# Kernel tuning notes

Hardware: AMD Instinct MI355X
Metric: run time of the kernel (lower is better)

## Reference

```python
import jax, jax.numpy as jnp
import numpy as np
import math

D_MODEL = 256
D_STATE = 16
D_CONV = 4
EXPAND = 2
N_HEADS = 4
D_INNER = EXPAND * D_MODEL          # 512
DT_RANK = (D_MODEL + 15) // 16      # 16
B_SZ, SEQ = 4, 2048


def setup_inputs() -> dict:
    key = jax.random.key(0)
    ks = jax.random.split(key, 12)
    rn = lambda i, shp, sc=0.02: jax.random.normal(ks[i], shp, dtype=jnp.float32) * sc
    x = jax.random.normal(ks[0], (B_SZ, SEQ, D_MODEL), dtype=jnp.float32)
    return dict(
        x=x,
        ln_g=jnp.ones((D_MODEL,), jnp.float32),
        ln_b=jnp.zeros((D_MODEL,), jnp.float32),
        W_in=rn(1, (D_MODEL, 2 * D_INNER)),
        conv_w=rn(2, (D_INNER, D_CONV), 0.1),
        conv_b=jnp.zeros((D_INNER,), jnp.float32),
        W_xproj=rn(3, (D_INNER, DT_RANK + 2 * D_STATE)),
        W_dt=rn(4, (DT_RANK, D_INNER), 0.1),
        b_dt=jnp.full((D_INNER,), -4.6, jnp.float32),  # softplus ~ 0.01 init
        A_log=jnp.log(jnp.tile(jnp.arange(1, D_STATE + 1, dtype=jnp.float32), (D_INNER, 1))),
        Dp=jnp.ones((D_INNER,), jnp.float32),
        W_out_m=rn(5, (D_INNER, D_MODEL)),
        W_qkv=rn(6, (D_MODEL, 3 * D_MODEL)),
        b_qkv=jnp.zeros((3 * D_MODEL,), jnp.float32),
        W_o=rn(7, (D_MODEL, D_MODEL)),
        b_o=jnp.zeros((D_MODEL,), jnp.float32),
        W_gate=rn(8, (2 * D_MODEL, D_MODEL)),
        b_gate=jnp.zeros((D_MODEL,), jnp.float32),
    )


def _sssd_forward(x, ln_g, ln_b, W_in, conv_w, conv_b, W_xproj, W_dt, b_dt,
                  A_log, Dp, W_out_m, W_qkv, b_qkv, W_o, b_o, W_gate, b_gate):
    B, L, D = x.shape
    # LayerNorm
    mu = x.mean(-1, keepdims=True)
    var = x.var(-1, keepdims=True)
    xn = (x - mu) * jax.lax.rsqrt(var + 1e-5) * ln_g + ln_b

    # ---- Mamba branch ----
    xz = xn @ W_in                      # (B,L,2*D_INNER)
    xm, z = jnp.split(xz, 2, axis=-1)
    # causal depthwise conv1d (kernel D_CONV)
    xp = jnp.pad(xm, ((0, 0), (D_CONV - 1, 0), (0, 0)))
    xc = conv_b + sum(xp[:, k:k + L, :] * conv_w[:, k] for k in range(D_CONV))
    xc = jax.nn.silu(xc)
    dbl = xc @ W_xproj                  # (B,L,DT_RANK+2*D_STATE)
    dt_in = dbl[..., :DT_RANK]
    Bm = dbl[..., DT_RANK:DT_RANK + D_STATE]
    Cm = dbl[..., DT_RANK + D_STATE:]
    dt = jax.nn.softplus(dt_in @ W_dt + b_dt)   # (B,L,D_INNER)
    A = -jnp.exp(A_log)                 # (D_INNER, D_STATE)

    def step(h, inp):
        x_t, dt_t, B_t, C_t = inp       # (B,Din),(B,Din),(B,N),(B,N)
        dA = jnp.exp(dt_t[..., None] * A)               # (B,Din,N)
        h = dA * h + (dt_t * x_t)[..., None] * B_t[:, None, :]
        y = jnp.einsum('bdn,bn->bd', h, C_t)
        return h, y

    h0 = jnp.zeros((B, D_INNER, D_STATE), x.dtype)
    xs = (jnp.swapaxes(xc, 0, 1), jnp.swapaxes(dt, 0, 1),
          jnp.swapaxes(Bm, 0, 1), jnp.swapaxes(Cm, 0, 1))
    _, ys = jax.lax.scan(step, h0, xs)
    y = jnp.swapaxes(ys, 0, 1) + xc * Dp
    y = y * jax.nn.silu(z)
    ssm_out = y @ W_out_m               # (B,L,D)

    # ---- MHSA branch (eval: no dropout) ----
    hd = D // N_HEADS
    qkv = xn @ W_qkv + b_qkv
    q, k, v = jnp.split(qkv, 3, axis=-1)
    sh = lambda t: t.reshape(B, L, N_HEADS, hd).transpose(0, 2, 1, 3)
    q, k, v = sh(q), sh(k), sh(v)
    scores = jnp.einsum('bhqd,bhkd->bhqk', q, k) * (1.0 / math.sqrt(hd))
    attn = jax.nn.softmax(scores, axis=-1)
    o = jnp.einsum('bhqk,bhkd->bhqd', attn, v).transpose(0, 2, 1, 3).reshape(B, L, D)
    attn_out = o @ W_o + b_o

    # ---- sigmoid gate fusion ----
    gate = jax.nn.sigmoid(jnp.concatenate([ssm_out, attn_out], axis=-1) @ W_gate + b_gate)
    fused = gate * ssm_out + (1.0 - gate) * attn_out
    return x + fused


def reference(x, ln_g, ln_b, W_in, conv_w, conv_b, W_xproj, W_dt, b_dt,
              A_log, Dp, W_out_m, W_qkv, b_qkv, W_o, b_o, W_gate, b_gate):
    return _sssd_forward(x, ln_g, ln_b, W_in, conv_w, conv_b, W_xproj, W_dt, b_dt,
                         A_log, Dp, W_out_m, W_qkv, b_qkv, W_o, b_o, W_gate, b_gate)
```

## Files before the change

### kernel.cpp

```cpp
#include <hip/hip_runtime.h>
#include <math.h>

#define B_SZ 4
#define SEQ 2048
#define DM 256
#define DI 512
#define DS 16
#define DTR 16
#define NH 4
#define HD 64
#define T_TOK (B_SZ*SEQ)
#define NCH 64
#define CL (SEQ/NCH)
#define QSCALE 0.18033688f

typedef short bf16x8 __attribute__((ext_vector_type(8)));
typedef float f32x4  __attribute__((ext_vector_type(4)));
typedef unsigned short u16;

__device__ __forceinline__ float sigmoidf_(float x){ return 1.f/(1.f+__expf(-x)); }
__device__ __forceinline__ u16 f2bf(float x){
  unsigned int u = __float_as_uint(x);
  u += 0x7fffu + ((u>>16)&1u);
  return (u16)(u>>16);
}
__device__ __forceinline__ float bf2f(u16 u){ return __uint_as_float(((unsigned)u)<<16); }
__device__ __forceinline__ unsigned cvt_pk_bf16(float lo, float hi){
  unsigned r;
  asm("v_cvt_pk_bf16_f32 %0, %1, %2" : "=v"(r) : "v"(lo), "v"(hi));
  return r;
}

struct TcvtArgs {
  const float* src[6];
  u16* dst[6];
  int K[6];
  int Nvalid[6];
  int Npad[6];
};
__global__ __launch_bounds__(256) void tcvt_all(TcvtArgs a) {
  int wi = blockIdx.z;
  int K = a.K[wi], Nv = a.Nvalid[wi], Np = a.Npad[wi];
  int k0 = blockIdx.x*64, n0 = blockIdx.y*64;
  if (k0 >= K || n0 >= Np) return;
  __shared__ u16 tile[64][65];
  const float* src = a.src[wi];
  u16* dst = a.dst[wi];
  int tn = threadIdx.x & 63, tq = threadIdx.x >> 6;
#pragma unroll
  for (int j=0;j<16;++j){
    int kk = j*4 + tq;
    int n = n0 + tn;
    tile[tn][kk] = (n < Nv) ? f2bf(src[(size_t)(k0+kk)*Nv + n]) : (u16)0;
  }
  __syncthreads();
#pragma unroll
  for (int j=0;j<16;++j){
    int nn = j*4 + tq;
    dst[(size_t)(n0+nn)*K + k0 + tn] = tile[nn][tn];
  }
}

__global__ __launch_bounds__(256) void ln_kernel(const float* __restrict__ x,
    const float* __restrict__ g, const float* __restrict__ b,
    u16* __restrict__ xn_bf) {
  int wid = threadIdx.x >> 6;
  int lane = threadIdx.x & 63;
  int token = blockIdx.x*4 + wid;
  const float* xr = x + (size_t)token*DM;
  float4 v = *(const float4*)&xr[lane*4];
  float s  = v.x+v.y+v.z+v.w;
  float ss = v.x*v.x+v.y*v.y+v.z*v.z+v.w*v.w;
  for (int m=1;m<64;m<<=1){ s += __shfl_xor(s,m); ss += __shfl_xor(ss,m); }
  float mu  = s * (1.f/DM);
  float var = ss*(1.f/DM) - mu*mu;
  float rs  = rsqrtf(var + 1e-5f);
  float4 gv = *(const float4*)&g[lane*4];
  float4 bv = *(const float4*)&b[lane*4];
  uint2 o;
  o.x = cvt_pk_bf16((v.x-mu)*rs*gv.x + bv.x, (v.y-mu)*rs*gv.y + bv.y);
  o.y = cvt_pk_bf16((v.z-mu)*rs*gv.z + bv.z, (v.w-mu)*rs*gv.w + bv.w);
  *(uint2*)&xn_bf[(size_t)token*DM + lane*4] = o;
}

template<int ACT>
__global__ __launch_bounds__(256) void gemm_mfma(const u16* __restrict__ A,
    const u16* __restrict__ Wt, const float* __restrict__ bias,
    float* __restrict__ C, u16* __restrict__ Cbf, int K, int ldc, int nvalid,
    int qcols, float qscale, const float* __restrict__ xres,
    const float* __restrict__ cat2, u16* __restrict__ vTout) {
  __shared__ u16 lds[12288];
  int tid = threadIdx.x;
  int m0 = blockIdx.y*128, n0 = blockIdx.x*64;
  int w = tid>>6, l = tid&63, lq = l&15, lg = l>>4;
  int wm = w>>1, wn = w&1;
  f32x4 acc[4][2] = {};
  for (int k0 = 0; k0 < K; k0 += 64) {
#pragma unroll
    for (int i=0;i<4;++i){
      int gid = i*256 + tid;
      int row = gid>>3, g = gid&7;
      *(bf16x8*)&lds[row*64 + ((g ^ (row&7))*8)] =
          *(const bf16x8*)&A[(size_t)(m0+row)*K + k0 + g*8];
    }
#pragma unroll
    for (int i=0;i<2;++i){
      int gid = i*256 + tid;
      int row = gid>>3, g = gid&7;
      *(bf16x8*)&lds[8192 + row*64 + ((g ^ (row&7))*8)] =
          *(const bf16x8*)&Wt[(size_t)(n0+row)*K + k0 + g*8];
    }
    __syncthreads();
#pragma unroll
    for (int ks=0;ks<2;++ks){
      bf16x8 af[4], bfv[2];
#pragma unroll
      for (int mi=0;mi<4;++mi){
        int row = wm*64 + mi*16 + lq;
        af[mi] = *(bf16x8*)&lds[row*64 + (((ks*4+lg) ^ (row&7))*8)];
      }
#pragma unroll
      for (int nj=0;nj<2;++nj){
        int row = wn*32 + nj*16 + lq;
        bfv[nj] = *(bf16x8*)&lds[8192 + row*64 + (((ks*4+lg) ^ (row&7))*8)];
      }
#pragma unroll
      for (int mi=0;mi<4;++mi)
#pragma unroll
        for (int nj=0;nj<2;++nj)
          acc[mi][nj] = __builtin_amdgcn_mfma_f32_16x16x32_bf16(af[mi], bfv[nj], acc[mi][nj], 0,0,0);
    }
    __syncthreads();
  }
#pragma unroll
  for (int mi=0;mi<4;++mi){
#pragma unroll
    for (int nj=0;nj<2;++nj){
#pragma unroll
      for (int r=0;r<4;++r){
        int row = m0 + wm*64 + mi*16 + lg*4 + r;
        int col = n0 + wn*32 + nj*16 + lq;
        if (col < nvalid) {
          float v = acc[mi][nj][r];
          if (bias) v += bias[col];
          if (col < qcols) v *= qscale;
          if (ACT==2) {
            float g = sigmoidf_(v);
            float sv = cat2[(size_t)row*512 + col];
            float av = cat2[(size_t)row*512 + 256 + col];
            C[(size_t)row*256 + col] = xres[(size_t)row*256 + col] + g*sv + (1.f-g)*av;
          } else if (ACT==3) {
            Cbf[(size_t)row*ldc + col] = f2bf(v);
            if (col >= 512) {
              int bb = row>>11, ll = row&2047;
              int hh = (col-512)>>6, dd = (col-512)&63;
              vTout[(((size_t)(bb*4+hh))*64 + dd)*SEQ + ll] = f2bf(v);
            }
          } else {
            if (ACT==1) v = sigmoidf_(v);
            if (C)   C[(size_t)row*ldc + col] = v;
            if (Cbf) Cbf[(size_t)row*ldc + col] = f2bf(v);
          }
        }
      }
    }
  }
}

__global__ __launch_bounds__(256) void conv_kernel(const u16* __restrict__ xzb,
    const float* __restrict__ cw, const float* __restrict__ cb,
    u16* __restrict__ xc_bf) {
  int idx = blockIdx.x*256 + threadIdx.x;
  int d2 = (idx & 255)*2;
  int t = idx >> 8;
  int l = t & (SEQ-1);
  float acc0 = cb[d2], acc1 = cb[d2+1];
  float4 wA = *(const float4*)&cw[d2*4];
  float4 wB = *(const float4*)&cw[d2*4+4];
  const u16* base = xzb + (size_t)t*1024 + d2;
  ushort2 v;
  if (l>=3){ v = *(const ushort2*)&base[-3*1024]; acc0 += bf2f(v.x)*wA.x; acc1 += bf2f(v.y)*wB.x; }
  if (l>=2){ v = *(const ushort2*)&base[-2*1024]; acc0 += bf2f(v.x)*wA.y; acc1 += bf2f(v.y)*wB.y; }
  if (l>=1){ v = *(const ushort2*)&base[-1*1024]; acc0 += bf2f(v.x)*wA.z; acc1 += bf2f(v.y)*wB.z; }
  v = *(const ushort2*)&base[0];
  acc0 += bf2f(v.x)*wA.w; acc1 += bf2f(v.y)*wB.w;
  float r0 = acc0 * sigmoidf_(acc0);
  float r1 = acc1 * sigmoidf_(acc1);
  *(unsigned*)&xc_bf[(size_t)t*DI + d2] = cvt_pk_bf16(r0, r1);
}

__global__ __launch_bounds__(256) void dt_kernel(const float* __restrict__ dbl,
    const float* __restrict__ Wdt, const float* __restrict__ bdt,
    float* __restrict__ dt) {
  __shared__ float sdbl[4][16];
  int wid = threadIdx.x>>6, lane = threadIdx.x&63;
  int token = blockIdx.x*4 + wid;
  if (lane < 16) sdbl[wid][lane] = dbl[(size_t)token*48 + lane];
  __syncthreads();
  float din[16];
#pragma unroll
  for (int k=0;k<16;++k) din[k] = sdbl[wid][k];
#pragma unroll
  for (int r=0;r<8;++r){
    int d = lane + r*64;
    float acc = bdt[d];
#pragma unroll
    for (int k=0;k<16;++k) acc += din[k]*Wdt[k*DI+d];
    float sp = (acc > 20.f) ? acc : log1pf(__expf(acc));
    dt[(size_t)token*DI+d] = sp;
  }
}

__global__ __launch_bounds__(512) void scan_p1(const u16* __restrict__ xc_bf,
    const float* __restrict__ dt, const float* __restrict__ dbl,
    const float* __restrict__ A_log, float* __restrict__ Pws, float* __restrict__ Hws) {
  __shared__ float sB[CL][16];
  int d = threadIdx.x;
  int bc = blockIdx.x;
  int b = bc >> 6, c = bc & 63;
  {
    int t = threadIdx.x >> 4, n = threadIdx.x & 15;
    sB[t][n] = dbl[((size_t)b*SEQ + c*CL + t)*48 + DTR + n];
  }
  __syncthreads();
  float An[16];
#pragma unroll
  for (int i=0;i<4;++i){
    float4 a = *(const float4*)&A_log[d*16 + i*4];
    An[i*4+0] = -__expf(a.x); An[i*4+1] = -__expf(a.y);
    An[i*4+2] = -__expf(a.z); An[i*4+3] = -__expf(a.w);
  }
  float h[16] = {};
  float P[16];
#pragma unroll
  for (int n=0;n<16;++n) P[n] = 1.f;
  size_t tok = (size_t)b*SEQ + c*CL;
  for (int t=0;t<CL;++t,++tok){
    float dtv = dt[tok*DI+d];
    float xcv = bf2f(xc_bf[tok*DI+d]);
    float u = dtv*xcv;
    float4 B0 = *(float4*)&sB[t][0];
    float4 B1 = *(float4*)&sB[t][4];
    float4 B2 = *(float4*)&sB[t][8];
    float4 B3 = *(float4*)&sB[t][12];
    float Bv[16] = {B0.x,B0.y,B0.z,B0.w,B1.x,B1.y,B1.z,B1.w,
                    B2.x,B2.y,B2.z,B2.w,B3.x,B3.y,B3.z,B3.w};
#pragma unroll
    for (int n=0;n<16;++n){
      float e = __expf(dtv*An[n]);
      P[n] *= e;
      h[n] = e*h[n] + u*Bv[n];
    }
  }
  size_t base = (((size_t)b*NCH + c)*DI + d)*16;
#pragma unroll
  for (int n=0;n<16;++n){ Pws[base+n] = P[n]; Hws[base+n] = h[n]; }
}

__global__ __launch_bounds__(256) void scan_combine(const float* __restrict__ Pws,
    const float* __restrict__ Hws, float* __restrict__ H0ws) {
  int gid = blockIdx.x*256 + threadIdx.x;
  int b  = gid >> 13;
  int dn = gid & 8191;
  float h0 = 0.f;
#pragma unroll 4
  for (int c=0;c<NCH;++c){
    size_t idx = ((size_t)(b*NCH+c)<<13) + dn;
    H0ws[idx] = h0;
    h0 = Pws[idx]*h0 + Hws[idx];
  }
}

__global__ __launch_bounds__(512) void scan_p2(const u16* __restrict__ xc_bf,
    const float* __restrict__ dt, const float* __restrict__ dbl,
    const float* __restrict__ A_log, const float* __restrict__ Dp,
    const u16* __restrict__ xzb, const float* __restrict__ H0ws,
    u16* __restrict__ ygate_bf) {
  __shared__ float sBC[CL][32];
  int d = threadIdx.x;
  int bc = blockIdx.x;
  int b = bc >> 6, c = bc & 63;
#pragma unroll
  for (int i=0;i<2;++i){
    int idx = i*512 + threadIdx.x;
    int t = idx >> 5, q = idx & 31;
    sBC[t][q] = dbl[((size_t)b*SEQ + c*CL + t)*48 + DTR + q];
  }
  __syncthreads();
  float An[16];
#pragma unroll
  for (int i=0;i<4;++i){
    float4 a = *(const float4*)&A_log[d*16 + i*4];
    An[i*4+0] = -__expf(a.x); An[i*4+1] = -__expf(a.y);
    An[i*4+2] = -__expf(a.z); An[i*4+3] = -__expf(a.w);
  }
  float Dd = Dp[d];
  float h[16];
  size_t base = (((size_t)b*NCH + c)*DI + d)*16;
#pragma unroll
  for (int i=0;i<4;++i){
    float4 h4 = *(const float4*)&H0ws[base + i*4];
    h[i*4+0]=h4.x; h[i*4+1]=h4.y; h[i*4+2]=h4.z; h[i*4+3]=h4.w;
  }
  size_t tok = (size_t)b*SEQ + c*CL;
  for (int t=0;t<CL;++t,++tok){
    float dtv = dt[tok*DI+d];
    float xcv = bf2f(xc_bf[tok*DI+d]);
    float zv  = bf2f(xzb[tok*1024 + DI + d]);
    float u = dtv*xcv;
    float4 B0 = *(float4*)&sBC[t][0];
    float4 B1 = *(float4*)&sBC[t][4];
    float4 B2 = *(float4*)&sBC[t][8];
    float4 B3 = *(float4*)&sBC[t][12];
    float4 C0 = *(float4*)&sBC[t][16];
    float4 C1 = *(float4*)&sBC[t][20];
    float4 C2 = *(float4*)&sBC[t][24];
    float4 C3 = *(float4*)&sBC[t][28];
    float Bv[16] = {B0.x,B0.y,B0.z,B0.w,B1.x,B1.y,B1.z,B1.w,
                    B2.x,B2.y,B2.z,B2.w,B3.x,B3.y,B3.z,B3.w};
    float Cv[16] = {C0.x,C0.y,C0.z,C0.w,C1.x,C1.y,C1.z,C1.w,
                    C2.x,C2.y,C2.z,C2.w,C3.x,C3.y,C3.z,C3.w};
    float y = 0.f;
#pragma unroll
    for (int n=0;n<16;++n){
      float e = __expf(dtv*An[n]);
      h[n] = e*h[n] + u*Bv[n];
      y += h[n]*Cv[n];
    }
    y += xcv*Dd;
    ygate_bf[tok*DI + d] = f2bf(y * (zv*sigmoidf_(zv)));
  }
}

__global__ __launch_bounds__(256) void attn_mfma_kernel(const u16* __restrict__ qkvb,
    const u16* __restrict__ vT,
    float* __restrict__ Opart, float* __restrict__ ml) {
  __shared__ u16 lds[24576];
  int H = blockIdx.x + 16*blockIdx.y + 256*(int)blockIdx.z;
  int cx = H & 7, k = H >> 3;
  int xq = k & 15;
  int G  = cx*8 + (k >> 4);
  int bh = G & 15, s = G >> 4;
  int b = bh>>2, h = bh&3;
  int tid = threadIdx.x;
  int w = tid>>6, l = tid&63;
  int lq = l & 15;
  int lg = l >> 4;
  size_t bbase = (size_t)b*SEQ;
  size_t vbase = (size_t)bh*HD*SEQ;
  int q0 = xq*128 + w*32;

  bf16x8 qf[2][2];
#pragma unroll
  for (int qg=0; qg<2; ++qg)
#pragma unroll
    for (int dsl=0; dsl<2; ++dsl)
      qf[qg][dsl] = *(const bf16x8*)&qkvb[(bbase + q0 + qg*16 + lq)*768 + h*HD + lg*8 + dsl*32];

  float m_[2] = {-1e30f,-1e30f}, l_[2] = {0.f,0.f};
  f32x4 oacc[2][4] = {};
  int pbase = 16384 + w*2048;

  int srow = tid>>3, sg = tid&7;
  int kt0 = s*8;
  bf16x8 kreg[2], vreg[2];

#define LOADT(kt) { \
  kreg[0] = *(const bf16x8*)&qkvb[(bbase + (size_t)(kt)*64 + srow)*768 + 256 + h*HD + sg*8]; \
  kreg[1] = *(const bf16x8*)&qkvb[(bbase + (size_t)(kt)*64 + srow + 32)*768 + 256 + h*HD + sg*8]; \
  vreg[0] = *(const bf16x8*)&vT[vbase + (size_t)srow*SEQ + (kt)*64 + sg*8]; \
  vreg[1] = *(const bf16x8*)&vT[vbase + (size_t)(srow+32)*SEQ + (kt)*64 + sg*8]; }
#define STORET(bi) { \
  *(bf16x8*)&lds[(bi)*4096 + srow*64 + ((sg ^ (srow&7))*8)] = kreg[0]; \
  *(bf16x8*)&lds[(bi)*4096 + (srow+32)*64 + ((sg ^ ((srow+32)&7))*8)] = kreg[1]; \
  *(bf16x8*)&lds[8192 + (bi)*4096 + srow*64 + ((sg ^ (srow&7))*8)] = vreg[0]; \
  *(bf16x8*)&lds[8192 + (bi)*4096 + (srow+32)*64 + ((sg ^ ((srow+32)&7))*8)] = vreg[1]; }

  LOADT(kt0);
  STORET(0);
  __syncthreads();
  int cur = 0;

  for (int it=0; it<8; ++it){
    if (it < 7) LOADT(kt0+it+1);

    int kb = cur*4096, vb = 8192 + cur*4096;
    f32x4 sacc[2][4] = {};
    __builtin_amdgcn_s_setprio(1);
#pragma unroll
    for (int kg=0;kg<4;++kg){
#pragma unroll
      for (int dsl=0;dsl<2;++dsl){
        int row = kg*16 + lq;
        bf16x8 kf = *(bf16x8*)&lds[kb + row*64 + (((dsl*4 + lg) ^ (row&7))*8)];
        sacc[0][kg] = __builtin_amdgcn_mfma_f32_16x16x32_bf16(kf, qf[0][dsl], sacc[0][kg], 0,0,0);
        sacc[1][kg] = __builtin_amdgcn_mfma_f32_16x16x32_bf16(kf, qf[1][dsl], sacc[1][kg], 0,0,0);
      }
    }
    __builtin_amdgcn_s_setprio(0);

#pragma unroll
    for (int qg=0;qg<2;++qg){
      float tm = sacc[qg][0][0];
#pragma unroll
      for (int kg=0;kg<4;++kg){
        float a = fmaxf(fmaxf(sacc[qg][kg][0],sacc[qg][kg][1]),
                        fmaxf(sacc[qg][kg][2],sacc[qg][kg][3]));
        tm = fmaxf(tm, a);
      }
      tm = fmaxf(tm, __shfl_xor(tm,16));
      tm = fmaxf(tm, __shfl_xor(tm,32));
      if (__any(tm - m_[qg] > 8.f)) {
        float mn = fmaxf(m_[qg], tm);
        float sc = exp2f(m_[qg] - mn);
        m_[qg] = mn;
        l_[qg] *= sc;
#pragma unroll
        for (int dg=0;dg<4;++dg){
          oacc[qg][dg][0]*=sc; oacc[qg][dg][1]*=sc; oacc[qg][dg][2]*=sc; oacc[qg][dg][3]*=sc;
        }
      }
      float ps = 0.f;
#pragma unroll
      for (int kg=0;kg<4;++kg){
        float p0 = exp2f(sacc[qg][kg][0] - m_[qg]);
        float p1 = exp2f(sacc[qg][kg][1] - m_[qg]);
        float p2 = exp2f(sacc[qg][kg][2] - m_[qg]);
        float p3 = exp2f(sacc[qg][kg][3] - m_[qg]);
        ps += (p0+p1)+(p2+p3);
        int off = pbase + qg*1024 + lq*64 + (((2*kg + (lg>>1)) ^ (lq&7))*8) + 4*(lg&1);
        *(unsigned*)&lds[off]   = cvt_pk_bf16(p0, p1);
        *(unsigned*)&lds[off+2] = cvt_pk_bf16(p2, p3);
      }
      ps += __shfl_xor(ps,16);
      ps += __shfl_xor(ps,32);
      l_[qg] += ps;
    }

    __builtin_amdgcn_s_setprio(1);
#pragma unroll
    for (int ks=0;ks<2;++ks){
      bf16x8 pf0 = *(bf16x8*)&lds[pbase        + lq*64 + (((ks*4 + lg) ^ (lq&7))*8)];
      bf16x8 pf1 = *(bf16x8*)&lds[pbase + 1024 + lq*64 + (((ks*4 + lg) ^ (lq&7))*8)];
#pragma unroll
      for (int dg=0;dg<4;++dg){
        int row = dg*16 + lq;
        bf16x8 vf = *(bf16x8*)&lds[vb + row*64 + (((ks*4 + lg) ^ (row&7))*8)];
        oacc[0][dg] = __builtin_amdgcn_mfma_f32_16x16x32_bf16(vf, pf0, oacc[0][dg], 0,0,0);
        oacc[1][dg] = __builtin_amdgcn_mfma_f32_16x16x32_bf16(vf, pf1, oacc[1][dg], 0,0,0);
      }
    }
    __builtin_amdgcn_s_setprio(0);

    if (it < 7) STORET(cur^1);
    __syncthreads();
    cur ^= 1;
  }
#undef LOADT
#undef STORET

  int sidx = bh*4 + s;
#pragma unroll
  for (int qg=0;qg<2;++qg){
    size_t rb = ((size_t)sidx*SEQ + q0 + qg*16 + lq)*64;
#pragma unroll
    for (int dg=0;dg<4;++dg)
#pragma unroll
      for (int r=0;r<4;++r)
        Opart[rb + dg*16 + lg*4 + r] = oacc[qg][dg][r];
    if (lg==0){
      ml[((size_t)sidx*SEQ + q0 + qg*16 + lq)*2    ] = m_[qg];
      ml[((size_t)sidx*SEQ + q0 + qg*16 + lq)*2 + 1] = l_[qg];
    }
  }
}

__global__ __launch_bounds__(256) void attn_merge_kernel(const float* __restrict__ Opart,
    const float* __restrict__ ml, u16* __restrict__ attn_bf) {
  int w = threadIdx.x>>6, lane = threadIdx.x&63;
  int R = blockIdx.x*4 + w;
  int bh = R>>11, q = R&2047;
  float m[4], lv[4];
#pragma unroll
  for (int s=0;s<4;++s){
    m[s]  = ml[((size_t)(bh*4+s)*SEQ + q)*2];
    lv[s] = ml[((size_t)(bh*4+s)*SEQ + q)*2 + 1];
  }
  float ms = fmaxf(fmaxf(m[0],m[1]),fmaxf(m[2],m[3]));
  float o = 0.f, lsum = 0.f;
#pragma unroll
  for (int s=0;s<4;++s){
    float wsc = exp2f(m[s]-ms);
    lsum += wsc*lv[s];
    o += wsc*Opart[((size_t)(bh*4+s)*SEQ + q)*64 + lane];
  }
  size_t token = (size_t)(bh>>2)*SEQ + q;
  attn_bf[token*DM + (bh&3)*HD + lane] = f2bf(o/lsum);
}

extern "C" void kernel_launch(void* const* d_in, const int* in_sizes, int n_in,
                              void* d_out, int out_size, void* d_ws, size_t ws_size,
                              hipStream_t stream) {
  const float* x      = (const float*)d_in[0];
  const float* ln_g   = (const float*)d_in[1];
  const float* ln_b   = (const float*)d_in[2];
  const float* W_in   = (const float*)d_in[3];
  const float* conv_w = (const float*)d_in[4];
  const float* conv_b = (const float*)d_in[5];
  const float* W_xproj= (const float*)d_in[6];
  const float* W_dt   = (const float*)d_in[7];
  const float* b_dt   = (const float*)d_in[8];
  const float* A_log  = (const float*)d_in[9];
  const float* Dp     = (const float*)d_in[10];
  const float* W_out_m= (const float*)d_in[11];
  const float* W_qkv  = (const float*)d_in[12];
  const float* b_qkv  = (const float*)d_in[13];
  const float* W_o    = (const float*)d_in[14];
  const float* b_o    = (const float*)d_in[15];
  const float* W_gate = (const float*)d_in[16];
  const float* b_gate = (const float*)d_in[17];
  float* out = (float*)d_out;

  float* ws = (float*)d_ws;
  u16*   xn_bf   = (u16*)(ws);
  u16*   xzb     = (u16*)(ws + 1048576);
  u16*   qkv_bf  = (u16*)(ws + 9437184);
  u16*   xc_bf   = (u16*)(ws + 12582912);
  float* dblb    = ws + 16777216;
  float* dtb     = ws + 17170432;
  u16*   ygate_bf= (u16*)(ws + 21364736);
  u16*   attn_bf = (u16*)(ws + 23461888);
  float* catb    = ws + 24510464;
  u16*   catb_bf = (u16*)(ws + 28704768);
  float* gateb   = ws + 30801920;
  u16*   Wt_all  = (u16*)(ws + 32899072);
  float* Opart = ws + 1048576;
  float* mlb   = (float*)xn_bf;
  u16*   vTb   = (u16*)gateb;
  float* Pws   = catb;
  float* Hws   = catb + 2097152;
  float* H0ws  = catb + 4194304;

  u16* Wt_in   = Wt_all;
  u16* Wt_qkv  = Wt_all + 262144;
  u16* Wt_out  = Wt_all + 458752;
  u16* Wt_o    = Wt_all + 589824;
  u16* Wt_gate = Wt_all + 655360;
  u16* Wt_xp   = Wt_all + 786432;

  TcvtArgs ta;
  ta.src[0]=W_in;    ta.dst[0]=Wt_in;   ta.K[0]=256; ta.Nvalid[0]=1024; ta.Npad[0]=1024;
  ta.src[1]=W_qkv;   ta.dst[1]=Wt_qkv;  ta.K[1]=256; ta.Nvalid[1]=768;  ta.Npad[1]=768;
  ta.src[2]=W_out_m; ta.dst[2]=Wt_out;  ta.K[2]=512; ta.Nvalid[2]=256;  ta.Npad[2]=256;
  ta.src[3]=W_o;     ta.dst[3]=Wt_o;    ta.K[3]=256; ta.Nvalid[3]=256;  ta.Npad[3]=256;
  ta.src[4]=W_gate;  ta.dst[4]=Wt_gate; ta.K[4]=512; ta.Nvalid[4]=256;  ta.Npad[4]=256;
  ta.src[5]=W_xproj; ta.dst[5]=Wt_xp;   ta.K[5]=512; ta.Nvalid[5]=48;   ta.Npad[5]=64;
  tcvt_all<<<dim3(8,16,6), 256, 0, stream>>>(ta);

  ln_kernel<<<T_TOK/4, 256, 0, stream>>>(x, ln_g, ln_b, xn_bf);
  gemm_mfma<0><<<dim3(16,64), 256, 0, stream>>>(xn_bf, Wt_in, nullptr, nullptr, xzb, 256, 1024, 1024, 0, 1.f, nullptr, nullptr, nullptr);
  gemm_mfma<3><<<dim3(12,64), 256, 0, stream>>>(xn_bf, Wt_qkv, b_qkv, nullptr, qkv_bf, 256, 768, 768, 256, QSCALE, nullptr, nullptr, vTb);
  conv_kernel<<<T_TOK, 256, 0, stream>>>(xzb, conv_w, conv_b, xc_bf);
  gemm_mfma<0><<<dim3(1,64), 256, 0, stream>>>(xc_bf, Wt_xp, nullptr, dblb, nullptr, 512, 48, 48, 0, 1.f, nullptr, nullptr, nullptr);
  dt_kernel<<<T_TOK/4, 256, 0, stream>>>(dblb, W_dt, b_dt, dtb);
  scan_p1<<<B_SZ*NCH, 512, 0, stream>>>(xc_bf, dtb, dblb, A_log, Pws, Hws);
  scan_combine<<<128, 256, 0, stream>>>(Pws, Hws, H0ws);
  scan_p2<<<B_SZ*NCH, 512, 0, stream>>>(xc_bf, dtb, dblb, A_log, Dp, xzb, H0ws, ygate_bf);
  attn_mfma_kernel<<<dim3(16, 16, 4), 256, 0, stream>>>(qkv_bf, vTb, Opart, mlb);
  attn_merge_kernel<<<8192, 256, 0, stream>>>(Opart, mlb, attn_bf);
  gemm_mfma<0><<<dim3(4,64), 256, 0, stream>>>(ygate_bf, Wt_out, nullptr, catb, catb_bf, 512, 512, 256, 0, 1.f, nullptr, nullptr, nullptr);
  gemm_mfma<0><<<dim3(4,64), 256, 0, stream>>>(attn_bf, Wt_o, b_o, catb+256, catb_bf+256, 256, 512, 256, 0, 1.f, nullptr, nullptr, nullptr);
  gemm_mfma<2><<<dim3(4,64), 256, 0, stream>>>(catb_bf, Wt_gate, b_gate, out, nullptr, 512, 256, 256, 0, 1.f, x, catb, nullptr);
}
```

Measured before the change: 252.5 us.

## Switch attention to 32x32x16 MFMA with register-resident P via lane exchange

The attention kernel moves from 16x16x32 to 32x32x16 bf16 MFMA tiles, with each wave owning 32 query rows. The softmax probabilities are repacked in registers through a cross-half shuffle instead of a round trip through LDS. K/V staging drops from double-buffered to single-buffered, which shrinks LDS use but adds an extra barrier per tile and loses overlap between stores and compute. The goal is fewer LDS accesses and MFMA instructions and possibly higher occupancy, at the risk of more sync stalls.

```diff
diff --git a/kernel.cpp b/kernel.cpp
--- a/kernel.cpp
+++ b/kernel.cpp
@@ -16,6 +16,7 @@
 
 typedef short bf16x8 __attribute__((ext_vector_type(8)));
 typedef float f32x4  __attribute__((ext_vector_type(4)));
+typedef float f32x16 __attribute__((ext_vector_type(16)));
 typedef unsigned short u16;
 
 __device__ __forceinline__ float sigmoidf_(float x){ return 1.f/(1.f+__expf(-x)); }
@@ -335,7 +336,7 @@
 __global__ __launch_bounds__(256) void attn_mfma_kernel(const u16* __restrict__ qkvb,
     const u16* __restrict__ vT,
     float* __restrict__ Opart, float* __restrict__ ml) {
-  __shared__ u16 lds[24576];
+  __shared__ u16 lds[8192];
   int H = blockIdx.x + 16*blockIdx.y + 256*(int)blockIdx.z;
   int cx = H & 7, k = H >> 3;
   int xq = k & 15;
@@ -344,22 +345,20 @@
   int b = bh>>2, h = bh&3;
   int tid = threadIdx.x;
   int w = tid>>6, l = tid&63;
-  int lq = l & 15;
-  int lg = l >> 4;
+  int lo32 = l & 31;
+  int hi = l >> 5;
   size_t bbase = (size_t)b*SEQ;
   size_t vbase = (size_t)bh*HD*SEQ;
   int q0 = xq*128 + w*32;
-
-  bf16x8 qf[2][2];
-#pragma unroll
-  for (int qg=0; qg<2; ++qg)
-#pragma unroll
-    for (int dsl=0; dsl<2; ++dsl)
-      qf[qg][dsl] = *(const bf16x8*)&qkvb[(bbase + q0 + qg*16 + lq)*768 + h*HD + lg*8 + dsl*32];
-
-  float m_[2] = {-1e30f,-1e30f}, l_[2] = {0.f,0.f};
-  f32x4 oacc[2][4] = {};
-  int pbase = 16384 + w*2048;
+  int q = q0 + lo32;
+
+  bf16x8 qf[4];
+#pragma unroll
+  for (int dsl=0; dsl<4; ++dsl)
+    qf[dsl] = *(const bf16x8*)&qkvb[(bbase + q)*768 + h*HD + dsl*16 + hi*8];
+
+  float m_ = -1e30f, l_ = 0.f;
+  f32x16 oacc[2] = {};
 
   int srow = tid>>3, sg = tid&7;
   int kt0 = s*8;
@@ -370,108 +369,99 @@
   kreg[1] = *(const bf16x8*)&qkvb[(bbase + (size_t)(kt)*64 + srow + 32)*768 + 256 + h*HD + sg*8]; \
   vreg[0] = *(const bf16x8*)&vT[vbase + (size_t)srow*SEQ + (kt)*64 + sg*8]; \
   vreg[1] = *(const bf16x8*)&vT[vbase + (size_t)(srow+32)*SEQ + (kt)*64 + sg*8]; }
-#define STORET(bi) { \
-  *(bf16x8*)&lds[(bi)*4096 + srow*64 + ((sg ^ (srow&7))*8)] = kreg[0]; \
-  *(bf16x8*)&lds[(bi)*4096 + (srow+32)*64 + ((sg ^ ((srow+32)&7))*8)] = kreg[1]; \
-  *(bf16x8*)&lds[8192 + (bi)*4096 + srow*64 + ((sg ^ (srow&7))*8)] = vreg[0]; \
-  *(bf16x8*)&lds[8192 + (bi)*4096 + (srow+32)*64 + ((sg ^ ((srow+32)&7))*8)] = vreg[1]; }
+#define STORET() { \
+  *(bf16x8*)&lds[srow*64 + ((sg ^ (srow&7))*8)] = kreg[0]; \
+  *(bf16x8*)&lds[(srow+32)*64 + ((sg ^ ((srow+32)&7))*8)] = kreg[1]; \
+  *(bf16x8*)&lds[4096 + srow*64 + ((sg ^ (srow&7))*8)] = vreg[0]; \
+  *(bf16x8*)&lds[4096 + (srow+32)*64 + ((sg ^ ((srow+32)&7))*8)] = vreg[1]; }
+#define EXCH(X, Y, s_own, s_oth) { \
+  unsigned give = (l < 32) ? (Y) : (X); \
+  unsigned got = __shfl_xor(give, 32); \
+  s_own = (l < 32) ? (X) : got; \
+  s_oth = (l < 32) ? got : (Y); }
 
   LOADT(kt0);
-  STORET(0);
-  __syncthreads();
-  int cur = 0;
-
   for (int it=0; it<8; ++it){
+    __syncthreads();
+    STORET();
+    __syncthreads();
     if (it < 7) LOADT(kt0+it+1);
 
-    int kb = cur*4096, vb = 8192 + cur*4096;
-    f32x4 sacc[2][4] = {};
-    __builtin_amdgcn_s_setprio(1);
-#pragma unroll
-    for (int kg=0;kg<4;++kg){
-#pragma unroll
-      for (int dsl=0;dsl<2;++dsl){
-        int row = kg*16 + lq;
-        bf16x8 kf = *(bf16x8*)&lds[kb + row*64 + (((dsl*4 + lg) ^ (row&7))*8)];
-        sacc[0][kg] = __builtin_amdgcn_mfma_f32_16x16x32_bf16(kf, qf[0][dsl], sacc[0][kg], 0,0,0);
-        sacc[1][kg] = __builtin_amdgcn_mfma_f32_16x16x32_bf16(kf, qf[1][dsl], sacc[1][kg], 0,0,0);
+#pragma unroll
+    for (int t32=0; t32<2; ++t32){
+      f32x16 sacc = {0,0,0,0,0,0,0,0,0,0,0,0,0,0,0,0};
+      __builtin_amdgcn_s_setprio(1);
+#pragma unroll
+      for (int dsl=0; dsl<4; ++dsl){
+        int row = t32*32 + lo32;
+        bf16x8 kf = *(bf16x8*)&lds[row*64 + (((dsl*2 + hi) ^ (row&7))*8)];
+        sacc = __builtin_amdgcn_mfma_f32_32x32x16_bf16(kf, qf[dsl], sacc, 0,0,0);
       }
-    }
-    __builtin_amdgcn_s_setprio(0);
-
-#pragma unroll
-    for (int qg=0;qg<2;++qg){
-      float tm = sacc[qg][0][0];
-#pragma unroll
-      for (int kg=0;kg<4;++kg){
-        float a = fmaxf(fmaxf(sacc[qg][kg][0],sacc[qg][kg][1]),
-                        fmaxf(sacc[qg][kg][2],sacc[qg][kg][3]));
-        tm = fmaxf(tm, a);
+      __builtin_amdgcn_s_setprio(0);
+
+      float tm = sacc[0];
+#pragma unroll
+      for (int r=1;r<16;++r) tm = fmaxf(tm, sacc[r]);
+      tm = fmaxf(tm, __shfl_xor(tm, 32));
+      if (__any(tm - m_ > 8.f)) {
+        float mn = fmaxf(m_, tm);
+        float sc = exp2f(m_ - mn);
+        m_ = mn;
+        l_ *= sc;
+#pragma unroll
+        for (int r=0;r<16;++r){ oacc[0][r] *= sc; oacc[1][r] *= sc; }
       }
-      tm = fmaxf(tm, __shfl_xor(tm,16));
-      tm = fmaxf(tm, __shfl_xor(tm,32));
-      if (__any(tm - m_[qg] > 8.f)) {
-        float mn = fmaxf(m_[qg], tm);
-        float sc = exp2f(m_[qg] - mn);
-        m_[qg] = mn;
-        l_[qg] *= sc;
-#pragma unroll
-        for (int dg=0;dg<4;++dg){
-          oacc[qg][dg][0]*=sc; oacc[qg][dg][1]*=sc; oacc[qg][dg][2]*=sc; oacc[qg][dg][3]*=sc;
-        }
+      float p[16];
+      float ps = 0.f;
+#pragma unroll
+      for (int r=0;r<16;++r){ p[r] = exp2f(sacc[r] - m_); ps += p[r]; }
+      ps += __shfl_xor(ps, 32);
+      l_ += ps;
+
+      unsigned A0 = cvt_pk_bf16(p[0],p[1]),  A1 = cvt_pk_bf16(p[2],p[3]);
+      unsigned B0 = cvt_pk_bf16(p[4],p[5]),  B1 = cvt_pk_bf16(p[6],p[7]);
+      unsigned C0 = cvt_pk_bf16(p[8],p[9]),  C1 = cvt_pk_bf16(p[10],p[11]);
+      unsigned D0 = cvt_pk_bf16(p[12],p[13]),D1 = cvt_pk_bf16(p[14],p[15]);
+      unsigned s0,s1,s2,s3,s4,s5,s6,s7;
+      EXCH(A0,B0,s0,s2); EXCH(A1,B1,s1,s3);
+      EXCH(C0,D0,s4,s6); EXCH(C1,D1,s5,s7);
+      bf16x8 pf0, pf1;
+      ((unsigned*)&pf0)[0]=s0; ((unsigned*)&pf0)[1]=s1; ((unsigned*)&pf0)[2]=s2; ((unsigned*)&pf0)[3]=s3;
+      ((unsigned*)&pf1)[0]=s4; ((unsigned*)&pf1)[1]=s5; ((unsigned*)&pf1)[2]=s6; ((unsigned*)&pf1)[3]=s7;
+
+      __builtin_amdgcn_s_setprio(1);
+#pragma unroll
+      for (int dtile=0; dtile<2; ++dtile){
+        int row = dtile*32 + lo32;
+        bf16x8 vf0 = *(bf16x8*)&lds[4096 + row*64 + (((t32*4 + 0 + hi) ^ (row&7))*8)];
+        bf16x8 vf1 = *(bf16x8*)&lds[4096 + row*64 + (((t32*4 + 2 + hi) ^ (row&7))*8)];
+        oacc[dtile] = __builtin_amdgcn_mfma_f32_32x32x16_bf16(vf0, pf0, oacc[dtile], 0,0,0);
+        oacc[dtile] = __builtin_amdgcn_mfma_f32_32x32x16_bf16(vf1, pf1, oacc[dtile], 0,0,0);
       }
-      float ps = 0.f;
-#pragma unroll
-      for (int kg=0;kg<4;++kg){
-        float p0 = exp2f(sacc[qg][kg][0] - m_[qg]);
-        float p1 = exp2f(sacc[qg][kg][1] - m_[qg]);
-        float p2 = exp2f(sacc[qg][kg][2] - m_[qg]);
-        float p3 = exp2f(sacc[qg][kg][3] - m_[qg]);
-        ps += (p0+p1)+(p2+p3);
-        int off = pbase + qg*1024 + lq*64 + (((2*kg + (lg>>1)) ^ (lq&7))*8) + 4*(lg&1);
-        *(unsigned*)&lds[off]   = cvt_pk_bf16(p0, p1);
-        *(unsigned*)&lds[off+2] = cvt_pk_bf16(p2, p3);
-      }
-      ps += __shfl_xor(ps,16);
-      ps += __shfl_xor(ps,32);
-      l_[qg] += ps;
-    }
-
-    __builtin_amdgcn_s_setprio(1);
-#pragma unroll
-    for (int ks=0;ks<2;++ks){
-      bf16x8 pf0 = *(bf16x8*)&lds[pbase        + lq*64 + (((ks*4 + lg) ^ (lq&7))*8)];
-      bf16x8 pf1 = *(bf16x8*)&lds[pbase + 1024 + lq*64 + (((ks*4 + lg) ^ (lq&7))*8)];
-#pragma unroll
-      for (int dg=0;dg<4;++dg){
-        int row = dg*16 + lq;
-        bf16x8 vf = *(bf16x8*)&lds[vb + row*64 + (((ks*4 + lg) ^ (row&7))*8)];
-        oacc[0][dg] = __builtin_amdgcn_mfma_f32_16x16x32_bf16(vf, pf0, oacc[0][dg], 0,0,0);
-        oacc[1][dg] = __builtin_amdgcn_mfma_f32_16x16x32_bf16(vf, pf1, oacc[1][dg], 0,0,0);
-      }
-    }
-    __builtin_amdgcn_s_setprio(0);
-
-    if (it < 7) STORET(cur^1);
-    __syncthreads();
-    cur ^= 1;
+      __builtin_amdgcn_s_setprio(0);
+    }
   }
 #undef LOADT
 #undef STORET
+#undef EXCH
 
   int sidx = bh*4 + s;
-#pragma unroll
-  for (int qg=0;qg<2;++qg){
-    size_t rb = ((size_t)sidx*SEQ + q0 + qg*16 + lq)*64;
-#pragma unroll
-    for (int dg=0;dg<4;++dg)
-#pragma unroll
-      for (int r=0;r<4;++r)
-        Opart[rb + dg*16 + lg*4 + r] = oacc[qg][dg][r];
-    if (lg==0){
-      ml[((size_t)sidx*SEQ + q0 + qg*16 + lq)*2    ] = m_[qg];
-      ml[((size_t)sidx*SEQ + q0 + qg*16 + lq)*2 + 1] = l_[qg];
-    }
+  size_t rb = ((size_t)sidx*SEQ + q)*64;
+#pragma unroll
+  for (int dtile=0; dtile<2; ++dtile){
+#pragma unroll
+    for (int rg=0; rg<4; ++rg){
+      float4 v4;
+      v4.x = oacc[dtile][rg*4+0];
+      v4.y = oacc[dtile][rg*4+1];
+      v4.z = oacc[dtile][rg*4+2];
+      v4.w = oacc[dtile][rg*4+3];
+      *(float4*)&Opart[rb + dtile*32 + rg*8 + 4*hi] = v4;
+    }
+  }
+  if (l < 32){
+    ml[((size_t)sidx*SEQ + q)*2    ] = m_;
+    ml[((size_t)sidx*SEQ + q)*2 + 1] = l_;
   }
 }
 
```

Measured after the change: 248.7 us. Within noise of the previous version (-1.5%).
